# Kernel optimization log

Measured on AMD Instinct MI355X. Metric: run time of the kernel, lower is better.

Reference implementation:

```python
import jax, jax.numpy as jnp
import numpy as np

N_EXPERTS = 8
TOP_K = 2


def setup_inputs() -> dict:
    key = jax.random.key(0)
    ks = jax.random.split(key, 5)
    B, T, C, E, H = 8, 2048, 256, 8, 682  # H = int(8/3*256)
    scale = 1.0 / np.sqrt(C)
    return {
        "x": jax.random.normal(ks[0], (B, T, C), dtype=jnp.float32),
        "router_w": jax.random.normal(ks[1], (E, C), dtype=jnp.float32) * scale,
        "w1": jax.random.normal(ks[2], (E, H, C), dtype=jnp.float32) * scale,
        "w2": jax.random.normal(ks[3], (E, C, H), dtype=jnp.float32) * (1.0 / np.sqrt(H)),
        "w3": jax.random.normal(ks[4], (E, H, C), dtype=jnp.float32) * scale,
    }


def reference(x, router_w, w1, w2, w3):
    B, T, C = x.shape
    flat = x.reshape(-1, C)  # [N, C]

    # Router: softmax over experts, top-k selection, renormalize.
    logits = flat @ router_w.T                     # [N, E]
    probs = jax.nn.softmax(logits, axis=-1)
    topk_probs, topk_idx = jax.lax.top_k(probs, TOP_K)
    topk_probs = topk_probs / (jnp.sum(topk_probs, axis=-1, keepdims=True) + 1e-9)

    # Dense gate matrix [N, E]: zero for non-selected experts (same math as
    # the masked loop, since unselected experts contribute weight 0).
    onehot = jax.nn.one_hot(topk_idx, N_EXPERTS, dtype=flat.dtype)  # [N, K, E]
    gates = jnp.einsum("nk,nke->ne", topk_probs, onehot)           # [N, E]

    # SwiGLU experts, computed densely over E and combined with gates.
    h1 = jnp.einsum("nc,ehc->neh", flat, w1)       # [N, E, H]
    h3 = jnp.einsum("nc,ehc->neh", flat, w3)       # [N, E, H]
    h = jax.nn.silu(h1) * h3                       # [N, E, H]
    y = jnp.einsum("neh,ech->nec", h, w2)          # [N, E, C]
    out = jnp.einsum("ne,nec->nc", gates, y)       # [N, C]
    return out.reshape(B, T, C)
```

## Files before the change

### kernel.cpp

```cpp
#include <hip/hip_runtime.h>
#include <hip/hip_bf16.h>

#define N_TOK 16384
#define C_DIM 256
#define E_NUM 8
#define H_DIM 682
#define H_PAD 768
#define NROWS (N_TOK * 2)
#define HB 64
#define APB (NROWS / HB)
#define MAXTILE 264

typedef short short8 __attribute__((ext_vector_type(8)));
typedef float floatx4 __attribute__((ext_vector_type(4)));
typedef unsigned int uint;

__device__ inline unsigned short f2bf(float v) {
    union { float f; uint u; } x; x.f = v;
    uint r = (x.u + 0x7fffu + ((x.u >> 16) & 1u)) >> 16;
    return (unsigned short)r;
}
__device__ inline float bf2f(unsigned short v) {
    union { uint u; float f; } x; x.u = ((uint)v) << 16; return x.f;
}

__device__ __forceinline__ void load_lds16(const void* g, void* l) {
    __builtin_amdgcn_global_load_lds(
        (const __attribute__((address_space(1))) unsigned int*)g,
        (__attribute__((address_space(3))) unsigned int*)l, 16, 0, 0);
}

#define VMCNT8 asm volatile("s_waitcnt vmcnt(8)" ::: "memory")
#define VMCNT6 asm volatile("s_waitcnt vmcnt(6)" ::: "memory")
#define VMCNT0 asm volatile("s_waitcnt vmcnt(0)" ::: "memory")
#define LGKM0  asm volatile("s_waitcnt lgkmcnt(0)" ::: "memory")

#define P13 (E_NUM * H_PAD * (C_DIM / 2))
#define P2  (E_NUM * C_DIM * (H_PAD / 2))
#define WCONV_BLKS ((2 * P13 + P2) / 256)

__global__ __launch_bounds__(256) void prep_kernel(
    const float* __restrict__ w1, const float* __restrict__ w3, const float* __restrict__ w2,
    unsigned short* __restrict__ w1b, unsigned short* __restrict__ w3b,
    unsigned short* __restrict__ w2b,
    const float* __restrict__ x, const float* __restrict__ rw,
    unsigned short* __restrict__ xb, int* __restrict__ as_e, float* __restrict__ as_gate) {
    __shared__ float rws[E_NUM * C_DIM];
    int tid = threadIdx.x;
    if (blockIdx.x < WCONV_BLKS) {
        int idx = blockIdx.x * 256 + tid;
        if (idx < 2 * P13) {
            const float* src = (idx < P13) ? w1 : w3;
            unsigned short* dst = (idx < P13) ? w1b : w3b;
            int i = (idx < P13) ? idx : idx - P13;
            int e = i / (H_PAD * (C_DIM / 2));
            int rem = i - e * (H_PAD * (C_DIM / 2));
            int r = rem / (C_DIM / 2);
            int c2 = rem - r * (C_DIM / 2);
            uint v = 0;
            if (r < H_DIM) {
                const float2 f = *(const float2*)(src + ((size_t)e * H_DIM + r) * C_DIM + c2 * 2);
                v = (uint)f2bf(f.x) | ((uint)f2bf(f.y) << 16);
            }
            ((uint*)dst)[i] = v;
        } else {
            int i = idx - 2 * P13;
            int e = i / (C_DIM * (H_PAD / 2));
            int rem = i - e * (C_DIM * (H_PAD / 2));
            int r = rem / (H_PAD / 2);
            int c2 = rem - r * (H_PAD / 2);
            uint v = 0;
            if (c2 * 2 < H_DIM) {
                const float2 f = *(const float2*)(w2 + ((size_t)e * C_DIM + r) * H_DIM + c2 * 2);
                v = (uint)f2bf(f.x) | ((uint)f2bf(f.y) << 16);
            }
            ((uint*)w2b)[i] = v;
        }
        return;
    }
    for (int i = tid; i < E_NUM * C_DIM; i += 256) rws[i] = rw[i];
    __syncthreads();
    int wave = tid >> 6, lane = tid & 63;
    int t = (blockIdx.x - WCONV_BLKS) * 4 + wave;
    const float4 xv = *(const float4*)(x + (size_t)t * C_DIM + lane * 4);
    uint2 pk;
    pk.x = (uint)f2bf(xv.x) | ((uint)f2bf(xv.y) << 16);
    pk.y = (uint)f2bf(xv.z) | ((uint)f2bf(xv.w) << 16);
    *(uint2*)(xb + (size_t)t * C_DIM + lane * 4) = pk;
    float p[E_NUM];
#pragma unroll
    for (int e = 0; e < E_NUM; e++) {
        const float* wr = &rws[e * C_DIM + lane * 4];
        p[e] = xv.x * wr[0] + xv.y * wr[1] + xv.z * wr[2] + xv.w * wr[3];
    }
#pragma unroll
    for (int off = 32; off >= 1; off >>= 1) {
#pragma unroll
        for (int e = 0; e < E_NUM; e++) p[e] += __shfl_down(p[e], off, 64);
    }
    if (lane == 0) {
        float m = p[0];
#pragma unroll
        for (int e = 1; e < E_NUM; e++) m = fmaxf(m, p[e]);
        float s = 0.f, q[E_NUM];
#pragma unroll
        for (int e = 0; e < E_NUM; e++) { q[e] = expf(p[e] - m); s += q[e]; }
#pragma unroll
        for (int e = 0; e < E_NUM; e++) q[e] /= s;
        int e0 = 0;
#pragma unroll
        for (int e = 1; e < E_NUM; e++) if (q[e] > q[e0]) e0 = e;
        int e1 = (e0 == 0) ? 1 : 0;
#pragma unroll
        for (int e = 0; e < E_NUM; e++) {
            if (e != e0 && q[e] > q[e1]) e1 = e;
        }
        float g0 = q[e0], g1 = q[e1];
        float denom = g0 + g1 + 1e-9f;
        g0 /= denom; g1 /= denom;
        as_e[t * 2] = e0; as_gate[t * 2] = g0;
        as_e[t * 2 + 1] = e1; as_gate[t * 2 + 1] = g1;
    }
}

__global__ __launch_bounds__(256) void hist_kernel(const int* __restrict__ as_e,
                                                   int* __restrict__ block_hist) {
    __shared__ int lh[E_NUM];
    int b = blockIdx.x, tid = threadIdx.x;
    if (tid < E_NUM) lh[tid] = 0;
    __syncthreads();
    for (int i = tid; i < APB; i += 256) atomicAdd(&lh[as_e[b * APB + i]], 1);
    __syncthreads();
    if (tid < E_NUM) block_hist[b * E_NUM + tid] = lh[tid];
}

__global__ void scan2_kernel(const int* __restrict__ block_hist, int* __restrict__ offsets,
                             int* __restrict__ block_base, int* __restrict__ tile_base) {
    __shared__ int tot[E_NUM], off[E_NUM];
    int e = threadIdx.x;
    if (e < E_NUM) {
        int s = 0;
        for (int b = 0; b < HB; b++) s += block_hist[b * E_NUM + e];
        tot[e] = s;
    }
    __syncthreads();
    if (e == 0) {
        int acc = 0;
        for (int i = 0; i < E_NUM; i++) { off[i] = acc; offsets[i] = acc; acc += tot[i]; }
        offsets[E_NUM] = acc;
        int t = 0;
        tile_base[0] = 0;
        for (int i = 0; i < E_NUM; i++) { t += (tot[i] + 127) / 128; tile_base[i + 1] = t; }
    }
    __syncthreads();
    if (e < E_NUM) {
        int acc = off[e];
        for (int b = 0; b < HB; b++) { block_base[b * E_NUM + e] = acc; acc += block_hist[b * E_NUM + e]; }
    }
}

__global__ __launch_bounds__(256) void scatter_kernel(
    const int* __restrict__ as_e, const int* __restrict__ block_base,
    int* __restrict__ row_token, int* __restrict__ as_row) {
    __shared__ int cur[E_NUM];
    int b = blockIdx.x, tid = threadIdx.x;
    if (tid < E_NUM) cur[tid] = block_base[b * E_NUM + tid];
    __syncthreads();
    for (int i = tid; i < APB; i += 256) {
        int a = b * APB + i;
        int e = as_e[a];
        int p = atomicAdd(&cur[e], 1);
        row_token[p] = a >> 1;
        as_row[a] = p;
    }
}

__device__ __forceinline__ int tile_to_expert(const int* __restrict__ tile_base, int bid) {
    int e = 0;
#pragma unroll
    for (int i = 1; i < E_NUM; i++) e += (bid >= tile_base[i]) ? 1 : 0;
    return e;
}

__global__ __launch_bounds__(256, 2) void expert_ffn1(
    const unsigned short* __restrict__ xb, const unsigned short* __restrict__ w1b,
    const unsigned short* __restrict__ w3b, const int* __restrict__ offsets,
    const int* __restrict__ tile_base, const int* __restrict__ row_token,
    unsigned short* __restrict__ h) {
    int bid = blockIdx.x;
    if (bid >= tile_base[E_NUM]) return;
    int e = tile_to_expert(tile_base, bid);
    int mt = bid - tile_base[e];
    int c = blockIdx.y;
    int off0 = offsets[e], off1 = offsets[e + 1];
    int row0 = off0 + mt * 128;
    int mval = min(128, off1 - row0);

    __shared__ union {
        unsigned short buf[2][12288];
        unsigned short Hs[128 * 136];
    } sm;

    int tid = threadIdx.x, lane = tid & 63, w = tid >> 6;
    int wm = w & 1, wn = w >> 1;
    int ra = tid >> 2;
    int acol = (((tid & 3) ^ ((ra >> 1) & 3))) * 8;
    int tok0 = row_token[row0 + min(ra, mval - 1)];
    int tok1 = row_token[row0 + min(ra + 64, mval - 1)];
    const unsigned short* a0p = xb + (size_t)tok0 * C_DIM + acol;
    const unsigned short* a1p = xb + (size_t)tok1 * C_DIM + acol;
    const unsigned short* b1p0 = w1b + ((size_t)e * H_PAD + c * 128 + ra) * C_DIM + acol;
    const unsigned short* b1p1 = b1p0 + (size_t)64 * C_DIM;
    const unsigned short* b3p0 = w3b + ((size_t)e * H_PAD + c * 128 + ra) * C_DIM + acol;
    const unsigned short* b3p1 = b3p0 + (size_t)64 * C_DIM;

    int wofs = w * 512;
    auto stage = [&](int kt, unsigned short* base) {
        int kb = kt * 32;
        load_lds16(a0p + kb, base + wofs);
        load_lds16(a1p + kb, base + 2048 + wofs);
        load_lds16(b1p0 + kb, base + 4096 + wofs);
        load_lds16(b1p1 + kb, base + 6144 + wofs);
        load_lds16(b3p0 + kb, base + 8192 + wofs);
        load_lds16(b3p1 + kb, base + 10240 + wofs);
    };

    int ko = ((lane >> 4) ^ ((lane >> 1) & 3)) * 8;
    int l15 = lane & 15;
    int arowf = wm * 64 + l15;
    int browf = wn * 64 + l15;
    int quad = lane >> 4;

    stage(0, sm.buf[0]);

    floatx4 acc1[4][4], acc3[4][4];
#pragma unroll
    for (int m = 0; m < 4; m++)
#pragma unroll
        for (int n = 0; n < 4; n++) {
            acc1[m][n] = (floatx4){0.f, 0.f, 0.f, 0.f};
            acc3[m][n] = (floatx4){0.f, 0.f, 0.f, 0.f};
        }

#pragma unroll
    for (int kt = 0; kt < 8; kt++) {
        if (kt + 1 < 8) stage(kt + 1, sm.buf[(kt + 1) & 1]);
        if (kt + 1 < 8) { VMCNT6; } else { VMCNT0; }
        __builtin_amdgcn_s_barrier();
        const unsigned short* cur = sm.buf[kt & 1];
        short8 af[4], b1f[4], b3f[4];
#pragma unroll
        for (int m = 0; m < 4; m++) af[m] = *(short8*)&cur[(arowf + m * 16) * 32 + ko];
#pragma unroll
        for (int n = 0; n < 4; n++) {
            b1f[n] = *(short8*)&cur[4096 + (browf + n * 16) * 32 + ko];
            b3f[n] = *(short8*)&cur[8192 + (browf + n * 16) * 32 + ko];
        }
        __builtin_amdgcn_s_setprio(1);
#pragma unroll
        for (int m = 0; m < 4; m++)
#pragma unroll
            for (int n = 0; n < 4; n++) {
                acc1[m][n] = __builtin_amdgcn_mfma_f32_16x16x32_bf16(af[m], b1f[n], acc1[m][n], 0, 0, 0);
                acc3[m][n] = __builtin_amdgcn_mfma_f32_16x16x32_bf16(af[m], b3f[n], acc3[m][n], 0, 0, 0);
            }
        __builtin_amdgcn_s_setprio(0);
        LGKM0;
        __builtin_amdgcn_s_barrier();
    }
    __syncthreads();

#pragma unroll
    for (int m = 0; m < 4; m++)
#pragma unroll
        for (int n = 0; n < 4; n++)
#pragma unroll
            for (int r = 0; r < 4; r++) {
                float h1 = acc1[m][n][r], h3 = acc3[m][n][r];
                float sv = h1 / (1.0f + __expf(-h1)) * h3;
                sm.Hs[(wm * 64 + m * 16 + quad * 4 + r) * 136 + wn * 64 + n * 16 + l15] = f2bf(sv);
            }
    __syncthreads();
#pragma unroll
    for (int it = 0; it < 8; it++) {
        int s = it * 256 + tid;
        int row = s >> 4, c16 = s & 15;
        if (row < mval)
            *(int4*)(h + (size_t)(row0 + row) * H_PAD + c * 128 + c16 * 8) =
                *(int4*)&sm.Hs[row * 136 + c16 * 8];
    }
}

__global__ __launch_bounds__(256, 2) void expert_ffn2(
    const unsigned short* __restrict__ h, const unsigned short* __restrict__ w2b,
    const int* __restrict__ offsets, const int* __restrict__ tile_base,
    unsigned short* __restrict__ y) {
    int bid = blockIdx.x;
    if (bid >= tile_base[E_NUM]) return;
    int e = tile_to_expert(tile_base, bid);
    int mt = bid - tile_base[e];
    int p = blockIdx.y;
    int off0 = offsets[e], off1 = offsets[e + 1];
    int row0 = off0 + mt * 128;
    int mval = min(128, off1 - row0);

    __shared__ union {
        unsigned short buf[2][16384];
        unsigned short Hs[128 * 136];
    } sm;

    int tid = threadIdx.x, lane = tid & 63, w = tid >> 6;
    int wm = w & 1, wn = w >> 1;
    int ra = tid >> 2;
    int acol = (((tid & 3) ^ ((ra >> 1) & 3))) * 8;
    const unsigned short* ap0 = h + (size_t)(row0 + ra) * H_PAD + acol;
    const unsigned short* ap1 = ap0 + (size_t)64 * H_PAD;
    const unsigned short* bp0 = w2b + ((size_t)e * C_DIM + p * 128 + ra) * H_PAD + acol;
    const unsigned short* bp1 = bp0 + (size_t)64 * H_PAD;

    int wofs = w * 512;
    auto stage = [&](int kt, unsigned short* base) {
        int kb = kt * 64;
#pragma unroll
        for (int kk = 0; kk < 2; kk++) {
            int ks = kb + kk * 32;
            unsigned short* b2 = base + kk * 8192;
            load_lds16(ap0 + ks, b2 + wofs);
            load_lds16(ap1 + ks, b2 + 2048 + wofs);
            load_lds16(bp0 + ks, b2 + 4096 + wofs);
            load_lds16(bp1 + ks, b2 + 6144 + wofs);
        }
    };

    int ko = ((lane >> 4) ^ ((lane >> 1) & 3)) * 8;
    int l15 = lane & 15;
    int arowf = wm * 64 + l15;
    int browf = wn * 64 + l15;
    int quad = lane >> 4;

    stage(0, sm.buf[0]);

    floatx4 acc[4][4];
#pragma unroll
    for (int m = 0; m < 4; m++)
#pragma unroll
        for (int n = 0; n < 4; n++) acc[m][n] = (floatx4){0.f, 0.f, 0.f, 0.f};

#pragma unroll
    for (int kt = 0; kt < H_PAD / 64; kt++) {
        if (kt + 1 < H_PAD / 64) stage(kt + 1, sm.buf[(kt + 1) & 1]);
        if (kt + 1 < H_PAD / 64) { VMCNT8; } else { VMCNT0; }
        __builtin_amdgcn_s_barrier();
        const unsigned short* cur = sm.buf[kt & 1];
#pragma unroll
        for (int kk = 0; kk < 2; kk++) {
            const unsigned short* c2 = cur + kk * 8192;
            short8 af[4], bf[4];
#pragma unroll
            for (int m = 0; m < 4; m++) af[m] = *(short8*)&c2[(arowf + m * 16) * 32 + ko];
#pragma unroll
            for (int n = 0; n < 4; n++) bf[n] = *(short8*)&c2[4096 + (browf + n * 16) * 32 + ko];
            __builtin_amdgcn_s_setprio(1);
#pragma unroll
            for (int m = 0; m < 4; m++)
#pragma unroll
                for (int n = 0; n < 4; n++)
                    acc[m][n] = __builtin_amdgcn_mfma_f32_16x16x32_bf16(af[m], bf[n], acc[m][n], 0, 0, 0);
            __builtin_amdgcn_s_setprio(0);
        }
        LGKM0;
        __builtin_amdgcn_s_barrier();
    }
    __syncthreads();

#pragma unroll
    for (int m = 0; m < 4; m++)
#pragma unroll
        for (int n = 0; n < 4; n++)
#pragma unroll
            for (int r = 0; r < 4; r++)
                sm.Hs[(wm * 64 + m * 16 + quad * 4 + r) * 136 + wn * 64 + n * 16 + l15] =
                    f2bf(acc[m][n][r]);
    __syncthreads();
#pragma unroll
    for (int it = 0; it < 8; it++) {
        int s = it * 256 + tid;
        int row = s >> 4, c16 = s & 15;
        if (row < mval)
            *(int4*)(y + (size_t)(row0 + row) * C_DIM + p * 128 + c16 * 8) =
                *(int4*)&sm.Hs[row * 136 + c16 * 8];
    }
}

__global__ __launch_bounds__(256) void combine_kernel(
    const unsigned short* __restrict__ y, const int* __restrict__ as_row,
    const float* __restrict__ as_gate, float* __restrict__ out) {
    int tid = threadIdx.x, lane = tid & 63;
    int t = blockIdx.x * 4 + (tid >> 6);
    int r0 = as_row[2 * t], r1 = as_row[2 * t + 1];
    float g0 = as_gate[2 * t], g1 = as_gate[2 * t + 1];
    uint2 a = *(const uint2*)(y + (size_t)r0 * C_DIM + lane * 4);
    uint2 b = *(const uint2*)(y + (size_t)r1 * C_DIM + lane * 4);
    float4 o;
    o.x = g0 * bf2f((unsigned short)(a.x & 0xffff)) + g1 * bf2f((unsigned short)(b.x & 0xffff));
    o.y = g0 * bf2f((unsigned short)(a.x >> 16)) + g1 * bf2f((unsigned short)(b.x >> 16));
    o.z = g0 * bf2f((unsigned short)(a.y & 0xffff)) + g1 * bf2f((unsigned short)(b.y & 0xffff));
    o.w = g0 * bf2f((unsigned short)(a.y >> 16)) + g1 * bf2f((unsigned short)(b.y >> 16));
    *(float4*)(out + (size_t)t * C_DIM + lane * 4) = o;
}

extern "C" void kernel_launch(void* const* d_in, const int* in_sizes, int n_in,
                              void* d_out, int out_size, void* d_ws, size_t ws_size,
                              hipStream_t stream) {
    const float* x = (const float*)d_in[0];
    const float* rw = (const float*)d_in[1];
    const float* w1 = (const float*)d_in[2];
    const float* w2 = (const float*)d_in[3];
    const float* w3 = (const float*)d_in[4];
    float* out = (float*)d_out;

    char* ws = (char*)d_ws;
    size_t o = 0;
    auto alloc = [&](size_t bytes) {
        void* p = ws + o;
        o = (o + bytes + 255) & ~(size_t)255;
        return p;
    };
    unsigned short* xb = (unsigned short*)alloc((size_t)N_TOK * C_DIM * 2);
    unsigned short* w1b = (unsigned short*)alloc((size_t)E_NUM * H_PAD * C_DIM * 2);
    unsigned short* w3b = (unsigned short*)alloc((size_t)E_NUM * H_PAD * C_DIM * 2);
    unsigned short* w2b = (unsigned short*)alloc((size_t)E_NUM * C_DIM * H_PAD * 2);
    unsigned short* hbuf = (unsigned short*)alloc((size_t)(NROWS + 128) * H_PAD * 2);
    unsigned short* ybuf = (unsigned short*)alloc((size_t)NROWS * C_DIM * 2);
    int* offsets = (int*)alloc((E_NUM + 1) * 4);
    int* tile_base = (int*)alloc((E_NUM + 1) * 4);
    int* as_e = (int*)alloc(NROWS * 4);
    float* as_gate = (float*)alloc(NROWS * 4);
    int* row_token = (int*)alloc(NROWS * 4);
    int* as_row = (int*)alloc(NROWS * 4);
    int* block_hist = (int*)alloc(HB * E_NUM * 4);
    int* block_base = (int*)alloc(HB * E_NUM * 4);

    prep_kernel<<<WCONV_BLKS + N_TOK / 4, 256, 0, stream>>>(
        w1, w3, w2, w1b, w3b, w2b, x, rw, xb, as_e, as_gate);
    hist_kernel<<<HB, 256, 0, stream>>>(as_e, block_hist);
    scan2_kernel<<<1, 64, 0, stream>>>(block_hist, offsets, block_base, tile_base);
    scatter_kernel<<<HB, 256, 0, stream>>>(as_e, block_base, row_token, as_row);

    expert_ffn1<<<dim3(MAXTILE, 6), 256, 0, stream>>>(xb, w1b, w3b, offsets, tile_base,
                                                      row_token, hbuf);
    expert_ffn2<<<dim3(MAXTILE, 2), 256, 0, stream>>>(hbuf, w2b, offsets, tile_base, ybuf);
    combine_kernel<<<N_TOK / 4, 256, 0, stream>>>(ybuf, as_row, as_gate, out);
}
```

Measured before the change: 187.6 us.

## Fuse gated combine into expert_ffn2 epilogue via atomic scatter-add to output

Removes the bf16 y intermediate buffer and the separate combine kernel. ffn2 now multiplies each accumulator by the row's gate and atomically adds it into the fp32 output at the owning token. The output is zeroed in extra prep_kernel blocks, and the scatter kernel now writes per-row gates. This trades a kernel launch and a y round-trip for many scalar fp32 global atomics with strided access, and the accumulation order becomes nondeterministic.

Measured after the change: 200.4 us. 1.07x slower.

```diff
diff --git a/kernel.cpp b/kernel.cpp
--- a/kernel.cpp
+++ b/kernel.cpp
@@ -38,13 +38,15 @@
 #define P13 (E_NUM * H_PAD * (C_DIM / 2))
 #define P2  (E_NUM * C_DIM * (H_PAD / 2))
 #define WCONV_BLKS ((2 * P13 + P2) / 256)
+#define ZERO_BLKS (N_TOK * C_DIM / (256 * 4))
 
 __global__ __launch_bounds__(256) void prep_kernel(
     const float* __restrict__ w1, const float* __restrict__ w3, const float* __restrict__ w2,
     unsigned short* __restrict__ w1b, unsigned short* __restrict__ w3b,
     unsigned short* __restrict__ w2b,
     const float* __restrict__ x, const float* __restrict__ rw,
-    unsigned short* __restrict__ xb, int* __restrict__ as_e, float* __restrict__ as_gate) {
+    unsigned short* __restrict__ xb, int* __restrict__ as_e, float* __restrict__ as_gate,
+    float* __restrict__ out) {
     __shared__ float rws[E_NUM * C_DIM];
     int tid = threadIdx.x;
     if (blockIdx.x < WCONV_BLKS) {
@@ -78,10 +80,15 @@
         }
         return;
     }
+    if (blockIdx.x < WCONV_BLKS + ZERO_BLKS) {
+        int i = (blockIdx.x - WCONV_BLKS) * 256 + tid;
+        ((float4*)out)[i] = (float4){0.f, 0.f, 0.f, 0.f};
+        return;
+    }
     for (int i = tid; i < E_NUM * C_DIM; i += 256) rws[i] = rw[i];
     __syncthreads();
     int wave = tid >> 6, lane = tid & 63;
-    int t = (blockIdx.x - WCONV_BLKS) * 4 + wave;
+    int t = (blockIdx.x - WCONV_BLKS - ZERO_BLKS) * 4 + wave;
     const float4 xv = *(const float4*)(x + (size_t)t * C_DIM + lane * 4);
     uint2 pk;
     pk.x = (uint)f2bf(xv.x) | ((uint)f2bf(xv.y) << 16);
@@ -161,7 +168,8 @@
 
 __global__ __launch_bounds__(256) void scatter_kernel(
     const int* __restrict__ as_e, const int* __restrict__ block_base,
-    int* __restrict__ row_token, int* __restrict__ as_row) {
+    const float* __restrict__ as_gate, int* __restrict__ row_token,
+    float* __restrict__ gate_row) {
     __shared__ int cur[E_NUM];
     int b = blockIdx.x, tid = threadIdx.x;
     if (tid < E_NUM) cur[tid] = block_base[b * E_NUM + tid];
@@ -171,7 +179,7 @@
         int e = as_e[a];
         int p = atomicAdd(&cur[e], 1);
         row_token[p] = a >> 1;
-        as_row[a] = p;
+        gate_row[p] = as_gate[a];
     }
 }
 
@@ -294,7 +302,8 @@
 __global__ __launch_bounds__(256, 2) void expert_ffn2(
     const unsigned short* __restrict__ h, const unsigned short* __restrict__ w2b,
     const int* __restrict__ offsets, const int* __restrict__ tile_base,
-    unsigned short* __restrict__ y) {
+    const int* __restrict__ row_token, const float* __restrict__ gate_row,
+    float* __restrict__ out) {
     int bid = blockIdx.x;
     if (bid >= tile_base[E_NUM]) return;
     int e = tile_to_expert(tile_base, bid);
@@ -304,10 +313,7 @@
     int row0 = off0 + mt * 128;
     int mval = min(128, off1 - row0);
 
-    __shared__ union {
-        unsigned short buf[2][16384];
-        unsigned short Hs[128 * 136];
-    } sm;
+    __shared__ unsigned short buf[2][16384];
 
     int tid = threadIdx.x, lane = tid & 63, w = tid >> 6;
     int wm = w & 1, wn = w >> 1;
@@ -338,7 +344,7 @@
     int browf = wn * 64 + l15;
     int quad = lane >> 4;
 
-    stage(0, sm.buf[0]);
+    stage(0, buf[0]);
 
     floatx4 acc[4][4];
 #pragma unroll
@@ -348,10 +354,10 @@
 
 #pragma unroll
     for (int kt = 0; kt < H_PAD / 64; kt++) {
-        if (kt + 1 < H_PAD / 64) stage(kt + 1, sm.buf[(kt + 1) & 1]);
+        if (kt + 1 < H_PAD / 64) stage(kt + 1, buf[(kt + 1) & 1]);
         if (kt + 1 < H_PAD / 64) { VMCNT8; } else { VMCNT0; }
         __builtin_amdgcn_s_barrier();
-        const unsigned short* cur = sm.buf[kt & 1];
+        const unsigned short* cur = buf[kt & 1];
 #pragma unroll
         for (int kk = 0; kk < 2; kk++) {
             const unsigned short* c2 = cur + kk * 8192;
@@ -371,42 +377,23 @@
         LGKM0;
         __builtin_amdgcn_s_barrier();
     }
-    __syncthreads();
-
-#pragma unroll
-    for (int m = 0; m < 4; m++)
-#pragma unroll
-        for (int n = 0; n < 4; n++)
-#pragma unroll
-            for (int r = 0; r < 4; r++)
-                sm.Hs[(wm * 64 + m * 16 + quad * 4 + r) * 136 + wn * 64 + n * 16 + l15] =
-                    f2bf(acc[m][n][r]);
-    __syncthreads();
-#pragma unroll
-    for (int it = 0; it < 8; it++) {
-        int s = it * 256 + tid;
-        int row = s >> 4, c16 = s & 15;
-        if (row < mval)
-            *(int4*)(y + (size_t)(row0 + row) * C_DIM + p * 128 + c16 * 8) =
-                *(int4*)&sm.Hs[row * 136 + c16 * 8];
-    }
-}
-
-__global__ __launch_bounds__(256) void combine_kernel(
-    const unsigned short* __restrict__ y, const int* __restrict__ as_row,
-    const float* __restrict__ as_gate, float* __restrict__ out) {
-    int tid = threadIdx.x, lane = tid & 63;
-    int t = blockIdx.x * 4 + (tid >> 6);
-    int r0 = as_row[2 * t], r1 = as_row[2 * t + 1];
-    float g0 = as_gate[2 * t], g1 = as_gate[2 * t + 1];
-    uint2 a = *(const uint2*)(y + (size_t)r0 * C_DIM + lane * 4);
-    uint2 b = *(const uint2*)(y + (size_t)r1 * C_DIM + lane * 4);
-    float4 o;
-    o.x = g0 * bf2f((unsigned short)(a.x & 0xffff)) + g1 * bf2f((unsigned short)(b.x & 0xffff));
-    o.y = g0 * bf2f((unsigned short)(a.x >> 16)) + g1 * bf2f((unsigned short)(b.x >> 16));
-    o.z = g0 * bf2f((unsigned short)(a.y & 0xffff)) + g1 * bf2f((unsigned short)(b.y & 0xffff));
-    o.w = g0 * bf2f((unsigned short)(a.y >> 16)) + g1 * bf2f((unsigned short)(b.y >> 16));
-    *(float4*)(out + (size_t)t * C_DIM + lane * 4) = o;
+
+#pragma unroll
+    for (int m = 0; m < 4; m++) {
+#pragma unroll
+        for (int r = 0; r < 4; r++) {
+            int row = wm * 64 + m * 16 + quad * 4 + r;
+            if (row < mval) {
+                int grow = row0 + row;
+                int token = row_token[grow];
+                float g = gate_row[grow];
+                float* obase = out + (size_t)token * C_DIM + p * 128 + wn * 64 + l15;
+#pragma unroll
+                for (int n = 0; n < 4; n++)
+                    atomicAdd(obase + n * 16, acc[m][n][r] * g);
+            }
+        }
+    }
 }
 
 extern "C" void kernel_launch(void* const* d_in, const int* in_sizes, int n_in,
@@ -431,24 +418,23 @@
     unsigned short* w3b = (unsigned short*)alloc((size_t)E_NUM * H_PAD * C_DIM * 2);
     unsigned short* w2b = (unsigned short*)alloc((size_t)E_NUM * C_DIM * H_PAD * 2);
     unsigned short* hbuf = (unsigned short*)alloc((size_t)(NROWS + 128) * H_PAD * 2);
-    unsigned short* ybuf = (unsigned short*)alloc((size_t)NROWS * C_DIM * 2);
     int* offsets = (int*)alloc((E_NUM + 1) * 4);
     int* tile_base = (int*)alloc((E_NUM + 1) * 4);
     int* as_e = (int*)alloc(NROWS * 4);
     float* as_gate = (float*)alloc(NROWS * 4);
     int* row_token = (int*)alloc(NROWS * 4);
-    int* as_row = (int*)alloc(NROWS * 4);
+    float* gate_row = (float*)alloc(NROWS * 4);
     int* block_hist = (int*)alloc(HB * E_NUM * 4);
     int* block_base = (int*)alloc(HB * E_NUM * 4);
 
-    prep_kernel<<<WCONV_BLKS + N_TOK / 4, 256, 0, stream>>>(
-        w1, w3, w2, w1b, w3b, w2b, x, rw, xb, as_e, as_gate);
+    prep_kernel<<<WCONV_BLKS + ZERO_BLKS + N_TOK / 4, 256, 0, stream>>>(
+        w1, w3, w2, w1b, w3b, w2b, x, rw, xb, as_e, as_gate, out);
     hist_kernel<<<HB, 256, 0, stream>>>(as_e, block_hist);
     scan2_kernel<<<1, 64, 0, stream>>>(block_hist, offsets, block_base, tile_base);
-    scatter_kernel<<<HB, 256, 0, stream>>>(as_e, block_base, row_token, as_row);
+    scatter_kernel<<<HB, 256, 0, stream>>>(as_e, block_base, as_gate, row_token, gate_row);
 
     expert_ffn1<<<dim3(MAXTILE, 6), 256, 0, stream>>>(xb, w1b, w3b, offsets, tile_base,
                                                       row_token, hbuf);
-    expert_ffn2<<<dim3(MAXTILE, 2), 256, 0, stream>>>(hbuf, w2b, offsets, tile_base, ybuf);
-    combine_kernel<<<N_TOK / 4, 256, 0, stream>>>(ybuf, as_row, as_gate, out);
-}
+    expert_ffn2<<<dim3(MAXTILE, 2), 256, 0, stream>>>(hbuf, w2b, offsets, tile_base,
+                                                      row_token, gate_row, out);
+}
```
